# Kernel optimization log

Measured on AMD Instinct MI355X. Metric: run time of the kernel, lower is better.

The kernel has to match this reference:

```python
import jax, jax.numpy as jnp
import numpy as np

N_HEADS = 16


def setup_inputs() -> dict:
    key = jax.random.key(0)
    ks = jax.random.split(key, 11)
    B, S, D = 4, 2048, 1024
    scale = 1.0 / np.sqrt(D)
    inp = {
        "xq": jax.random.normal(ks[0], (B, S, D), jnp.float32),
        "xk": jax.random.normal(ks[1], (B, S, D), jnp.float32),
        "xv": jax.random.normal(ks[2], (B, S, D), jnp.float32),
        "wq": jax.random.normal(ks[3], (D, D), jnp.float32) * scale,
        "bq": jnp.zeros((D,), jnp.float32),
        "wk": jax.random.normal(ks[4], (D, D), jnp.float32) * scale,
        "bk": jnp.zeros((D,), jnp.float32),
        "wv": jax.random.normal(ks[5], (D, D), jnp.float32) * scale,
        "bv": jnp.zeros((D,), jnp.float32),
        "wo": jax.random.normal(ks[6], (D, D), jnp.float32) * scale,
        "bo": jnp.zeros((D,), jnp.float32),
    }
    return inp


def reference(xq, xk, xv, wq, bq, wk, bk, wv, bv, wo, bo):
    B, S, D = xq.shape
    H = N_HEADS
    dh = D // H

    def split_heads(x):
        # (B, S, D) -> (B, H, S, dh)
        return x.reshape(B, S, H, dh).transpose(0, 2, 1, 3)

    q = split_heads(xq @ wq + bq)
    k = split_heads(xk @ wk + bk)
    v = split_heads(xv @ wv + bv)

    # FFT-based autocorrelation along the sequence axis (axis=2)
    q_fft = jnp.fft.rfft(q, axis=2)
    k_fft = jnp.fft.rfft(k, axis=2)
    autocorr = jnp.fft.irfft(q_fft * jnp.conj(k_fft), n=S, axis=2)  # (B,H,S,dh)
    scaled = autocorr / jnp.sqrt(jnp.float32(dh))

    # top-k delay selection over mean correlation across channel dim
    k_top = max(S // 5, 1)
    mean_corr = scaled.mean(axis=-1)  # (B,H,S)
    top_values, top_indices = jax.lax.top_k(mean_corr, k_top)  # (B,H,K)

    # gather values at top delays: (B,H,K,dh)
    v_sel = jnp.take_along_axis(v, top_indices[..., None], axis=2)
    weights = jax.nn.softmax(top_values, axis=-1)  # (B,H,K)
    attended = jnp.einsum('bhk,bhkd->bhd', weights, v_sel)  # (B,H,dh)

    # broadcast across seq, merge heads, output projection
    out = jnp.broadcast_to(attended[:, :, None, :], (B, H, S, dh))
    out = out.transpose(0, 2, 1, 3).reshape(B, S, D)
    return out @ wo + bo
```

## Files before the change

kernel.cpp:

```cpp
#include <hip/hip_runtime.h>
#include <math.h>

#define SB 4
#define SS 2048
#define SD 1024
#define SH 16
#define KTOP 409
#define KSL 8
#define KPS 52

typedef float f32x4  __attribute__((ext_vector_type(4)));
typedef short bf16x8 __attribute__((ext_vector_type(8)));
typedef short s16x4  __attribute__((ext_vector_type(4)));

__device__ __forceinline__ short f2bf(float x) {
  unsigned u = __float_as_uint(x);
  u += 0x7fff + ((u >> 16) & 1);
  return (short)(u >> 16);
}
__device__ __forceinline__ float bf2f(short s) {
  return __uint_as_float(((unsigned)(unsigned short)s) << 16);
}

__device__ __forceinline__ void gld16(const void* g, void* l) {
  __builtin_amdgcn_global_load_lds(
      (const __attribute__((address_space(1))) void*)g,
      (__attribute__((address_space(3))) void*)l, 16, 0, 0);
}

#define XS(i) ((i) ^ (((i) >> 4) & 15))

template<int SIGN>
__device__ __forceinline__ void fft2048_lds(float2* z, const float2* tw, int tid) {
#pragma unroll
  for (int l = 0; l < 4; ++l) {
    int bf = tid + l * 256;
    int i0 = XS(2 * bf), i1 = XS(2 * bf + 1);
    float2 a = z[i0], b = z[i1];
    z[i0] = make_float2(a.x + b.x, a.y + b.y);
    z[i1] = make_float2(a.x - b.x, a.y - b.y);
  }
  __syncthreads();
#pragma unroll
  for (int lq = 1; lq <= 9; lq += 2) {
    const int q = 1 << lq;
#pragma unroll
    for (int l = 0; l < 2; ++l) {
      int bf = tid + l * 256;
      int p = bf & (q - 1);
      int base = ((bf >> lq) << (lq + 2)) + p;
      int e1 = p << (9 - lq);
      int e2 = e1 << 1;
      int e3 = e1 * 3;
      float2 w1 = tw[XS(e1)];
      float2 w2 = tw[XS(e2)];
      float s3 = 1.f; int e3w = e3;
      if (e3 >= 1024) { e3w = e3 - 1024; s3 = -1.f; }
      float2 w3 = tw[XS(e3w)]; w3.x *= s3; w3.y *= s3;
      float2 t0 = z[XS(base)];
      float2 vb = z[XS(base + 2 * q)];
      float2 vc = z[XS(base + q)];
      float2 vd = z[XS(base + 3 * q)];
      float w1i = SIGN * w1.y, w2i = SIGN * w2.y, w3i = SIGN * w3.y;
      float2 t1 = make_float2(vb.x * w1.x - vb.y * w1i, vb.x * w1i + vb.y * w1.x);
      float2 t2 = make_float2(vc.x * w2.x - vc.y * w2i, vc.x * w2i + vc.y * w2.x);
      float2 t3 = make_float2(vd.x * w3.x - vd.y * w3i, vd.x * w3i + vd.y * w3.x);
      float2 s02 = make_float2(t0.x + t2.x, t0.y + t2.y);
      float2 d02 = make_float2(t0.x - t2.x, t0.y - t2.y);
      float2 s13 = make_float2(t1.x + t3.x, t1.y + t3.y);
      float2 d13 = make_float2(t1.x - t3.x, t1.y - t3.y);
      float2 r13 = make_float2(SIGN * d13.y, -SIGN * d13.x);
      z[XS(base)]         = make_float2(s02.x + s13.x, s02.y + s13.y);
      z[XS(base + q)]     = make_float2(d02.x + r13.x, d02.y + r13.y);
      z[XS(base + 2 * q)] = make_float2(s02.x - s13.x, s02.y - s13.y);
      z[XS(base + 3 * q)] = make_float2(d02.x - r13.x, d02.y - r13.y);
    }
    __syncthreads();
  }
}

template<int SIGN>
__device__ __forceinline__ void fft2048x2_lds(
    float2* __restrict__ z0, float2* __restrict__ z1,
    const float2* tw, int tid)
{
#pragma unroll
  for (int l = 0; l < 4; ++l) {
    int bf = tid + l * 256;
    int i0 = XS(2 * bf), i1 = XS(2 * bf + 1);
    float2 a0 = z0[i0], b0 = z0[i1];
    float2 a1 = z1[i0], b1 = z1[i1];
    z0[i0] = make_float2(a0.x + b0.x, a0.y + b0.y);
    z0[i1] = make_float2(a0.x - b0.x, a0.y - b0.y);
    z1[i0] = make_float2(a1.x + b1.x, a1.y + b1.y);
    z1[i1] = make_float2(a1.x - b1.x, a1.y - b1.y);
  }
  __syncthreads();
#pragma unroll
  for (int lq = 1; lq <= 9; lq += 2) {
    const int q = 1 << lq;
#pragma unroll
    for (int l = 0; l < 2; ++l) {
      int bf = tid + l * 256;
      int p = bf & (q - 1);
      int base = ((bf >> lq) << (lq + 2)) + p;
      int e1 = p << (9 - lq);
      int e2 = e1 << 1;
      int e3 = e1 * 3;
      float2 w1 = tw[XS(e1)];
      float2 w2 = tw[XS(e2)];
      float s3 = 1.f; int e3w = e3;
      if (e3 >= 1024) { e3w = e3 - 1024; s3 = -1.f; }
      float2 w3 = tw[XS(e3w)]; w3.x *= s3; w3.y *= s3;
      float w1i = SIGN * w1.y, w2i = SIGN * w2.y, w3i = SIGN * w3.y;
      const int ia = XS(base), ib = XS(base + 2 * q),
                ic = XS(base + q), id = XS(base + 3 * q);
#pragma unroll
      for (int s = 0; s < 2; ++s) {
        float2* z = s ? z1 : z0;
        float2 t0 = z[ia];
        float2 vb = z[ib];
        float2 vc = z[ic];
        float2 vd = z[id];
        float2 t1 = make_float2(vb.x * w1.x - vb.y * w1i, vb.x * w1i + vb.y * w1.x);
        float2 t2 = make_float2(vc.x * w2.x - vc.y * w2i, vc.x * w2i + vc.y * w2.x);
        float2 t3 = make_float2(vd.x * w3.x - vd.y * w3i, vd.x * w3i + vd.y * w3.x);
        float2 s02 = make_float2(t0.x + t2.x, t0.y + t2.y);
        float2 d02 = make_float2(t0.x - t2.x, t0.y - t2.y);
        float2 s13 = make_float2(t1.x + t3.x, t1.y + t3.y);
        float2 d13 = make_float2(t1.x - t3.x, t1.y - t3.y);
        float2 r13 = make_float2(SIGN * d13.y, -SIGN * d13.x);
        z[ia] = make_float2(s02.x + s13.x, s02.y + s13.y);
        z[ic] = make_float2(d02.x + r13.x, d02.y + r13.y);
        z[ib] = make_float2(s02.x - s13.x, s02.y - s13.y);
        z[id] = make_float2(d02.x - r13.x, d02.y - r13.y);
      }
    }
    __syncthreads();
  }
}

__global__ __launch_bounds__(256) void twiddle_k(float2* __restrict__ twtab) {
  int j = blockIdx.x * 256 + threadIdx.x;
  float a = 6.2831853071795864769f * (float)j / 2048.0f;
  twtab[j] = make_float2(cosf(a), -sinf(a));
}

__global__ __launch_bounds__(256) void splitwt_k(
    const float* __restrict__ wq, const float* __restrict__ wk,
    short* __restrict__ wqt, short* __restrict__ wkt)
{
  const float* W = blockIdx.z ? wk : wq;
  short* Wt = blockIdx.z ? wkt : wqt;
  const int n0 = blockIdx.x * 64, k0 = blockIdx.y * 64;
  __shared__ float T[64][65];
  const int tid = threadIdx.x;
#pragma unroll
  for (int l = 0; l < 4; ++l) {
    int idx = tid + l * 256;
    int r = idx >> 4, c4 = (idx & 15) << 2;
    float4 v = *(const float4*)&W[(size_t)(k0 + r) * SD + n0 + c4];
    T[r][c4 + 0] = v.x; T[r][c4 + 1] = v.y; T[r][c4 + 2] = v.z; T[r][c4 + 3] = v.w;
  }
  __syncthreads();
#pragma unroll
  for (int l = 0; l < 4; ++l) {
    int idx = tid + l * 256;
    int nr = idx >> 4, k4 = (idx & 15) << 2;
    s16x4 hi, lo;
#pragma unroll
    for (int j = 0; j < 4; ++j) {
      float x = T[k4 + j][nr];
      short hb = f2bf(x);
      hi[j] = hb; lo[j] = f2bf(x - bf2f(hb));
    }
    int ks = (((k4 >> 3) ^ (nr & 7)) << 3) | (k4 & 7);
    *(s16x4*)&Wt[(size_t)(n0 + nr) * 2048 + k0 + ks] = hi;
    *(s16x4*)&Wt[(size_t)(n0 + nr) * 2048 + 1024 + k0 + ks] = lo;
  }
}

__global__ __launch_bounds__(256) void splitx2_k(
    const float* __restrict__ Xq, const float* __restrict__ Xk,
    short* __restrict__ Xqh, short* __restrict__ Xql,
    short* __restrict__ Xkh, short* __restrict__ Xkl)
{
  const int tid = threadIdx.x;
  const int row = blockIdx.x * 2 + (tid >> 7);
  const int G = tid & 127;
  const float* X = blockIdx.y ? Xk : Xq;
  short* Xh = blockIdx.y ? Xkh : Xqh;
  short* Xl = blockIdx.y ? Xkl : Xql;
  const float* src = X + ((size_t)row << 10) + (G << 3);
  float4 a = *(const float4*)src;
  float4 b = *(const float4*)(src + 4);
  float xs[8] = {a.x, a.y, a.z, a.w, b.x, b.y, b.z, b.w};
  bf16x8 hi, lo;
#pragma unroll
  for (int j = 0; j < 8; ++j) {
    short hb = f2bf(xs[j]);
    hi[j] = hb; lo[j] = f2bf(xs[j] - bf2f(hb));
  }
  int Gd = (G & 0x78) | ((G ^ row) & 7);
  size_t d = ((size_t)row << 10) + (Gd << 3);
  *(bf16x8*)&Xh[d] = hi;
  *(bf16x8*)&Xl[d] = lo;
}

__global__ __launch_bounds__(256) void projm_k(
    const short* __restrict__ Xh, const short* __restrict__ Xl,
    const short* __restrict__ Wt, const float* __restrict__ bias,
    float* __restrict__ Out, int ldT)
{
  const int n0 = blockIdx.x * 128, m0 = blockIdx.y * 128;
  __shared__ __align__(16) short Ah[128 * 64];
  __shared__ __align__(16) short Al[128 * 64];
  __shared__ __align__(16) short Bh[128 * 64];
  __shared__ __align__(16) short Bl[128 * 64];
  const int tid = threadIdx.x;
  const int wave = tid >> 6, lane = tid & 63, l15 = lane & 15, kq = lane >> 4;
  const int wr = wave >> 1, wc = wave & 1;
  const int sr = lane >> 3, sc = lane & 7;
  f32x4 acc[4][4];
#pragma unroll
  for (int i = 0; i < 4; ++i)
#pragma unroll
    for (int j = 0; j < 4; ++j)
#pragma unroll
      for (int r = 0; r < 4; ++r) acc[i][j][r] = 0.f;
  float bval[4];
#pragma unroll
  for (int j = 0; j < 4; ++j) bval[j] = bias[n0 + wc * 64 + j * 16 + l15];

  for (int s = 0; s < 16; ++s) {
    __syncthreads();
#pragma unroll
    for (int l = 0; l < 4; ++l) {
      int rr = l * 32 + wave * 8 + sr;
      int lofs = (l * 32 + wave * 8) * 64;
      size_t gA = ((size_t)(m0 + rr) << 10) + (s << 6) + (sc << 3);
      gld16(Xh + gA, Ah + lofs);
      gld16(Xl + gA, Al + lofs);
      size_t gB = ((size_t)(n0 + rr) << 11) + (s << 6) + (sc << 3);
      gld16(Wt + gB, Bh + lofs);
      gld16(Wt + gB + 1024, Bl + lofs);
    }
    __syncthreads();
#pragma unroll
    for (int ks = 0; ks < 2; ++ks) {
      int seg = ks * 4 + kq;
      bf16x8 ah[4], al[4], bh[4], bl[4];
#pragma unroll
      for (int i = 0; i < 4; ++i) {
        int ar = wr * 64 + i * 16 + l15;
        int addr = ar * 64 + ((seg ^ (ar & 7)) << 3);
        ah[i] = *(const bf16x8*)&Ah[addr];
        al[i] = *(const bf16x8*)&Al[addr];
      }
#pragma unroll
      for (int j = 0; j < 4; ++j) {
        int br = wc * 64 + j * 16 + l15;
        int addr = br * 64 + ((seg ^ (br & 7)) << 3);
        bh[j] = *(const bf16x8*)&Bh[addr];
        bl[j] = *(const bf16x8*)&Bl[addr];
      }
#pragma unroll
      for (int i = 0; i < 4; ++i)
#pragma unroll
        for (int j = 0; j < 4; ++j) {
          acc[i][j] = __builtin_amdgcn_mfma_f32_16x16x32_bf16(ah[i], bh[j], acc[i][j], 0, 0, 0);
          acc[i][j] = __builtin_amdgcn_mfma_f32_16x16x32_bf16(al[i], bh[j], acc[i][j], 0, 0, 0);
          acc[i][j] = __builtin_amdgcn_mfma_f32_16x16x32_bf16(ah[i], bl[j], acc[i][j], 0, 0, 0);
        }
    }
  }
#pragma unroll
  for (int i = 0; i < 4; ++i)
#pragma unroll
    for (int j = 0; j < 4; ++j) {
      int n = n0 + wc * 64 + j * 16 + l15;
      int tb = m0 + wr * 64 + i * 16 + kq * 4;
      float4 v = make_float4(acc[i][j][0] + bval[j], acc[i][j][1] + bval[j],
                             acc[i][j][2] + bval[j], acc[i][j][3] + bval[j]);
      *(float4*)&Out[(size_t)n * ldT + tb] = v;
    }
}

__global__ __launch_bounds__(256) void fftcorr_k(
    const float* __restrict__ Qt, const float* __restrict__ Kt,
    float* __restrict__ P, const float2* __restrict__ twtab, int ld)
{
  const int dg = blockIdx.x, h = blockIdx.y, b = blockIdx.z;
  float* Pb = P + (size_t)b * SH * SS * 2;
  const size_t bofs = (size_t)b * SS;
  __shared__ float2 z0[2048];
  __shared__ float2 z1[2048];
  __shared__ float2 tw[1024];
  const int tid = threadIdx.x;
  for (int j = tid; j < 1024; j += 256) tw[XS(j)] = twtab[j];

  const int n = h * 64 + dg * 2;
  const float* q0 = Qt + (size_t)n * ld + bofs;
  const float* k0 = Kt + (size_t)n * ld + bofs;
  const float* q1 = q0 + ld;
  const float* k1 = k0 + ld;
#pragma unroll
  for (int l = 0; l < 8; ++l) {
    int t = tid + l * 256;
    int rv = __brev((unsigned)t) >> 21;
    z0[XS(rv)] = make_float2(q0[t], k0[t]);
    z1[XS(rv)] = make_float2(q1[t], k1[t]);
  }
  __syncthreads();
  fft2048x2_lds<1>(z0, z1, tw, tid);
#pragma unroll
  for (int l = 0; l < 8; ++l) {
    int f = tid + l * 256;
    int fc = (2048 - f) & 2047;
    float prr = 0.f, pii = 0.f;
#pragma unroll
    for (int s = 0; s < 2; ++s) {
      const float2* z = s ? z1 : z0;
      float2 Z = z[XS(f)];
      float2 Zc = z[XS(fc)];
      float Zcr = Zc.x, Zci = -Zc.y;
      float Qr = 0.5f * (Z.x + Zcr), Qi = 0.5f * (Z.y + Zci);
      float Kr = 0.5f * (Z.y - Zci), Ki = -0.5f * (Z.x - Zcr);
      prr += Qr * Kr + Qi * Ki;
      pii += Qi * Kr - Qr * Ki;
    }
    atomicAdd(&Pb[((size_t)h * SS + f) * 2 + 0], prr);
    atomicAdd(&Pb[((size_t)h * SS + f) * 2 + 1], pii);
  }
}

__global__ __launch_bounds__(256) void ifft_topk_k(
    const float* __restrict__ P, const float2* __restrict__ twtab,
    int* __restrict__ sidx, float* __restrict__ sw)
{
  const int bh = blockIdx.x;
  __shared__ float2 z[2048];
  __shared__ float2 tw[1024];
  __shared__ unsigned keys[2048];
  __shared__ int el_i[KTOP];
  __shared__ float el_w[KTOP];
  __shared__ int hist[256];
  __shared__ int scan_sh[256];
  __shared__ int cnt2, tiecnt, sel_v;
  __shared__ unsigned kmax_sh;
  __shared__ float Zsh;
  const int tid = threadIdx.x;
  const float SCL = 1.0f / (2048.0f * 512.0f);

  for (int j = tid; j < 1024; j += 256) tw[XS(j)] = twtab[j];
  if (tid == 0) { cnt2 = 0; tiecnt = 0; kmax_sh = 0u; Zsh = 0.f; }
#pragma unroll
  for (int l = 0; l < 8; ++l) {
    int f = tid + l * 256;
    int rv = __brev((unsigned)f) >> 21;
    z[XS(rv)] = make_float2(P[((size_t)bh * SS + f) * 2 + 0],
                            P[((size_t)bh * SS + f) * 2 + 1]);
  }
  __syncthreads();
  fft2048_lds<-1>(z, tw, tid);

  unsigned lm = 0u;
#pragma unroll
  for (int l = 0; l < 8; ++l) {
    int i = tid + l * 256;
    float v = z[XS(i)].x * SCL;
    z[XS(i)].x = v;
    unsigned u = __float_as_uint(v);
    unsigned k = (u & 0x80000000u) ? ~u : (u | 0x80000000u);
    keys[i] = k;
    lm = max(lm, k);
  }
  atomicMax(&kmax_sh, lm);
  __syncthreads();

  unsigned prefix = 0u;
  int remaining = KTOP;
  for (int p = 3; p >= 0; --p) {
    hist[tid] = 0;
    __syncthreads();
    unsigned mask_hi = (p == 3) ? 0u : (0xFFFFFFFFu << ((p + 1) * 8));
#pragma unroll
    for (int l = 0; l < 8; ++l) {
      unsigned k = keys[tid + l * 256];
      if ((k & mask_hi) == prefix) atomicAdd(&hist[(k >> (p * 8)) & 255], 1);
    }
    __syncthreads();
    scan_sh[tid] = hist[tid];
    __syncthreads();
    for (int off = 1; off < 256; off <<= 1) {
      int add = (tid + off < 256) ? scan_sh[tid + off] : 0;
      __syncthreads();
      scan_sh[tid] += add;
      __syncthreads();
    }
    if (scan_sh[tid] >= remaining && (tid == 255 || scan_sh[tid + 1] < remaining))
      sel_v = tid;
    __syncthreads();
    int v = sel_v;
    int above = (v == 255) ? 0 : scan_sh[v + 1];
    remaining -= above;
    prefix |= ((unsigned)v) << (p * 8);
    __syncthreads();
  }
  const unsigned T = prefix;
  unsigned km = kmax_sh;
  float vmax = __uint_as_float((km & 0x80000000u) ? (km ^ 0x80000000u) : ~km);

#pragma unroll
  for (int l = 0; l < 8; ++l) {
    int i = tid + l * 256;
    unsigned k = keys[i];
    if (k > T) {
      int pos = atomicAdd(&cnt2, 1);
      el_i[pos] = i;
      el_w[pos] = expf(z[XS(i)].x - vmax);
    } else if (k == T) {
      atomicAdd(&tiecnt, 1);
    }
  }
  __syncthreads();
  int need = KTOP - cnt2;
  if (tiecnt == need) {
#pragma unroll
    for (int l = 0; l < 8; ++l) {
      int i = tid + l * 256;
      if (keys[i] == T) {
        int pos = atomicAdd(&cnt2, 1);
        el_i[pos] = i;
        el_w[pos] = expf(z[XS(i)].x - vmax);
      }
    }
  } else if (tid == 0) {
    int pos = cnt2;
    for (int i = 0; i < SS && pos < KTOP; ++i)
      if (keys[i] == T) { el_i[pos] = i; el_w[pos] = expf(z[XS(i)].x - vmax); ++pos; }
  }
  __syncthreads();
  float zs = 0.f;
  for (int l = tid; l < KTOP; l += 256) zs += el_w[l];
  atomicAdd(&Zsh, zs);
  __syncthreads();
  float invZ = 1.0f / Zsh;
  for (int l = tid; l < KTOP; l += 256) {
    sidx[bh * KTOP + l] = el_i[l];
    sw[bh * KTOP + l]   = el_w[l] * invZ;
  }
}

__global__ __launch_bounds__(256) void xbar_k(
    const int* __restrict__ sidx, const float* __restrict__ sw,
    const float* __restrict__ xv, float* __restrict__ xbar)
{
  const int bh = blockIdx.x, b = bh >> 4, sl = blockIdx.y;
  const int r0 = sl * KPS;
  const int r1 = min(KTOP, r0 + KPS);
  __shared__ int il[KPS];
  __shared__ float wl[KPS];
  const int tid = threadIdx.x;
  if (tid < r1 - r0) {
    il[tid] = sidx[bh * KTOP + r0 + tid];
    wl[tid] = sw[bh * KTOP + r0 + tid];
  }
  __syncthreads();
  const float4* xv4 = (const float4*)xv;
  float4 acc = make_float4(0.f, 0.f, 0.f, 0.f);
  for (int r = 0; r < r1 - r0; ++r) {
    float w = wl[r];
    float4 v = xv4[(size_t)(b * SS + il[r]) * 256 + tid];
    acc.x += w * v.x; acc.y += w * v.y; acc.z += w * v.z; acc.w += w * v.w;
  }
  float* dst = xbar + (size_t)bh * 1024 + tid * 4;
  atomicAdd(dst + 0, acc.x); atomicAdd(dst + 1, acc.y);
  atomicAdd(dst + 2, acc.z); atomicAdd(dst + 3, acc.w);
}

__global__ __launch_bounds__(256) void initbias_k(
    const float* __restrict__ bv, const float* __restrict__ bo,
    float* __restrict__ att, float* __restrict__ orow)
{
  int i = blockIdx.x * 256 + threadIdx.x;
  if (i < 4096) att[i] = bv[i & 1023];
  else          orow[i - 4096] = bo[i & 1023];
}

__global__ __launch_bounds__(256) void attend_k(
    const float* __restrict__ xbar, const float* __restrict__ wv,
    float* __restrict__ att)
{
  const int b = blockIdx.y, i0 = blockIdx.x * 64;
  __shared__ float xs[16 * 64];
  const int tid = threadIdx.x;
#pragma unroll
  for (int l = 0; l < 4; ++l) {
    int f = tid + l * 256;
    xs[f] = xbar[(size_t)(b * 16 + (f >> 6)) * 1024 + i0 + (f & 63)];
  }
  __syncthreads();
  const float4* wv4 = (const float4*)wv;
  const int h = tid >> 4;
  float4 acc = make_float4(0.f, 0.f, 0.f, 0.f);
  for (int m = 0; m < 64; ++m) {
    float xvs = xs[h * 64 + m];
    float4 w = wv4[(size_t)(i0 + m) * 256 + tid];
    acc.x += xvs * w.x; acc.y += xvs * w.y; acc.z += xvs * w.z; acc.w += xvs * w.w;
  }
  float* dst = att + (size_t)b * 1024 + tid * 4;
  atomicAdd(dst + 0, acc.x); atomicAdd(dst + 1, acc.y);
  atomicAdd(dst + 2, acc.z); atomicAdd(dst + 3, acc.w);
}

__global__ __launch_bounds__(256) void oproj_k(
    const float* __restrict__ att, const float* __restrict__ wo,
    float* __restrict__ orow)
{
  const int b = blockIdx.y, m0 = blockIdx.x * 64;
  __shared__ float as_[64];
  const int tid = threadIdx.x;
  if (tid < 64) as_[tid] = att[(size_t)b * 1024 + m0 + tid];
  __syncthreads();
  const float4* wo4 = (const float4*)wo;
  float4 acc = make_float4(0.f, 0.f, 0.f, 0.f);
  for (int m = 0; m < 64; ++m) {
    float a = as_[m];
    float4 w = wo4[(size_t)(m0 + m) * 256 + tid];
    acc.x += a * w.x; acc.y += a * w.y; acc.z += a * w.z; acc.w += a * w.w;
  }
  float* dst = orow + (size_t)b * 1024 + tid * 4;
  atomicAdd(dst + 0, acc.x); atomicAdd(dst + 1, acc.y);
  atomicAdd(dst + 2, acc.z); atomicAdd(dst + 3, acc.w);
}

__global__ __launch_bounds__(256) void bcast_k(
    const float* __restrict__ orow, float* __restrict__ out)
{
  int idx = blockIdx.x * 256 + threadIdx.x;
  const float4* o4 = (const float4*)orow;
  ((float4*)out)[idx] = o4[((idx >> 19) << 8) | (idx & 255)];
}

extern "C" void kernel_launch(void* const* d_in, const int* in_sizes, int n_in,
                              void* d_out, int out_size, void* d_ws, size_t ws_size,
                              hipStream_t stream) {
  (void)in_sizes; (void)n_in; (void)out_size;
  const float* xq = (const float*)d_in[0];
  const float* xk = (const float*)d_in[1];
  const float* xv = (const float*)d_in[2];
  const float* wq = (const float*)d_in[3];
  const float* bq = (const float*)d_in[4];
  const float* wk = (const float*)d_in[5];
  const float* bk = (const float*)d_in[6];
  const float* wv = (const float*)d_in[7];
  const float* bv = (const float*)d_in[8];
  const float* wo = (const float*)d_in[9];
  const float* bo = (const float*)d_in[10];
  float* out = (float*)d_out;

  char* base = (char*)d_ws;
  float* P = (float*)base;
  size_t off = (size_t)SB * SH * SS * 2 * 4;
  float2* twtab = (float2*)(base + off); off += 1024 * 8;
  int*   sidx = (int*)  (base + off); off += (size_t)SB * SH * KTOP * 4;
  float* sw   = (float*)(base + off); off += (size_t)SB * SH * KTOP * 4;
  float* xbar = (float*)(base + off); off += (size_t)SB * SH * SD * 4;
  float* att  = (float*)(base + off); off += (size_t)SB * SD * 4;
  float* orow = (float*)(base + off); off += (size_t)SB * SD * 4;

  size_t big0 = (off + 1048575) & ~(size_t)1048575;
  const size_t SZ_X = (size_t)SB * SS * SD * 2;
  const size_t SZ_T = (size_t)SD * SB * SS * 4;
  const size_t SZ_W = (size_t)SD * 2048 * 2;
  size_t need_big = big0 + 4 * SZ_X + 2 * SZ_T + 2 * SZ_W;

  twiddle_k<<<dim3(4), 256, 0, stream>>>(twtab);
  hipMemsetAsync(P, 0, (size_t)SB * SH * SS * 2 * sizeof(float), stream);
  hipMemsetAsync(xbar, 0, (size_t)SB * SH * SD * sizeof(float), stream);

  if (ws_size >= need_big) {
    char* bb = base + big0;
    short* Xqh = (short*)(bb);
    short* Xql = (short*)(bb + SZ_X);
    short* Xkh = (short*)(bb + 2 * SZ_X);
    short* Xkl = (short*)(bb + 3 * SZ_X);
    float* Qt  = (float*)(bb + 4 * SZ_X);
    float* Kt  = (float*)(bb + 4 * SZ_X + SZ_T);
    short* Wqt = (short*)(bb + 4 * SZ_X + 2 * SZ_T);
    short* Wkt = (short*)(bb + 4 * SZ_X + 2 * SZ_T + SZ_W);

    splitwt_k<<<dim3(16, 16, 2), 256, 0, stream>>>(wq, wk, Wqt, Wkt);
    splitx2_k<<<dim3(SB * SS / 2, 2), 256, 0, stream>>>(xq, xk, Xqh, Xql, Xkh, Xkl);
    projm_k<<<dim3(8, SB * SS / 128), 256, 0, stream>>>(Xqh, Xql, Wqt, bq, Qt, SB * SS);
    projm_k<<<dim3(8, SB * SS / 128), 256, 0, stream>>>(Xkh, Xkl, Wkt, bk, Kt, SB * SS);
    fftcorr_k<<<dim3(32, 16, SB), 256, 0, stream>>>(Qt, Kt, P, twtab, SB * SS);
  } else {
    char* ob = (char*)d_out;
    float* Qt  = (float*)(ob);
    float* Kt  = (float*)(ob + ( 8u << 20));
    short* Wqt = (short*)(ob + (16u << 20));
    short* Wkt = (short*)(ob + (20u << 20));
    short* Xh  = (short*)(ob + (24u << 20));
    short* Xl  = (short*)(ob + (28u << 20));

    splitwt_k<<<dim3(16, 16, 2), 256, 0, stream>>>(wq, wk, Wqt, Wkt);
    for (int b = 0; b < SB; ++b) {
      const float* xqb = xq + (size_t)b * SS * SD;
      const float* xkb = xk + (size_t)b * SS * SD;
      splitx2_k<<<dim3(SS / 2, 1), 256, 0, stream>>>(xqb, xqb, Xh, Xl, Xh, Xl);
      projm_k<<<dim3(8, SS / 128), 256, 0, stream>>>(Xh, Xl, Wqt, bq, Qt, SS);
      splitx2_k<<<dim3(SS / 2, 1), 256, 0, stream>>>(xkb, xkb, Xh, Xl, Xh, Xl);
      projm_k<<<dim3(8, SS / 128), 256, 0, stream>>>(Xh, Xl, Wkt, bk, Kt, SS);
      fftcorr_k<<<dim3(32, 16, 1), 256, 0, stream>>>(
          Qt, Kt, P + (size_t)b * SH * SS * 2, twtab, SS);
    }
  }

  ifft_topk_k<<<dim3(SB * SH), 256, 0, stream>>>(P, twtab, sidx, sw);
  xbar_k<<<dim3(SB * SH, KSL), 256, 0, stream>>>(sidx, sw, xv, xbar);
  initbias_k<<<dim3(32), 256, 0, stream>>>(bv, bo, att, orow);
  attend_k<<<dim3(16, SB), 256, 0, stream>>>(xbar, wv, att);
  oproj_k<<<dim3(16, SB), 256, 0, stream>>>(att, wo, orow);
  bcast_k<<<dim3(8192), 256, 0, stream>>>(orow, out);
}
```

Baseline: 397.0 us.

## Batch Q/K projections, replace FFT atomics with partials, warp-shuffle scan

Merges the Q and K projection GEMMs into one launch using blockIdx.z. fftcorr now has each block process 8 channels instead of 2, with vectorized float2 loads, and writes per-group partial spectra that ifft_topk sums in place of global atomics. That also drops the P memset. The LDS swizzle gains a higher-bit XOR to cut bank conflicts, and the radix-select prefix scan uses wavefront shuffles instead of a barrier-heavy Hillis-Steele loop. The cost is fewer fftcorr blocks (lower parallelism) and an extra partial-spectrum buffer.

```diff
diff --git a/kernel.cpp b/kernel.cpp
--- a/kernel.cpp
+++ b/kernel.cpp
@@ -28,7 +28,7 @@
       (__attribute__((address_space(3))) void*)l, 16, 0, 0);
 }
 
-#define XS(i) ((i) ^ (((i) >> 4) & 15))
+#define XS(i) ((i) ^ ((((i) >> 4) ^ ((i) >> 8)) & 15))
 
 template<int SIGN>
 __device__ __forceinline__ void fft2048_lds(float2* z, const float2* tw, int tid) {
@@ -208,10 +208,16 @@
 }
 
 __global__ __launch_bounds__(256) void projm_k(
-    const short* __restrict__ Xh, const short* __restrict__ Xl,
-    const short* __restrict__ Wt, const float* __restrict__ bias,
-    float* __restrict__ Out, int ldT)
-{
+    const short* __restrict__ Xqh, const short* __restrict__ Xql,
+    const short* __restrict__ Wq_, const float* __restrict__ bq_,
+    float* __restrict__ Oq_,
+    const short* __restrict__ Xkh, const short* __restrict__ Xkl,
+    const short* __restrict__ Wk_, const float* __restrict__ bk_,
+    float* __restrict__ Ok_, int ldT)
+{
+  const short* Xh; const short* Xl; const short* Wt; const float* bias; float* Out;
+  if (blockIdx.z == 0) { Xh = Xqh; Xl = Xql; Wt = Wq_; bias = bq_; Out = Oq_; }
+  else                 { Xh = Xkh; Xl = Xkl; Wt = Wk_; bias = bk_; Out = Ok_; }
   const int n0 = blockIdx.x * 128, m0 = blockIdx.y * 128;
   __shared__ __align__(16) short Ah[128 * 64];
   __shared__ __align__(16) short Al[128 * 64];
@@ -288,54 +294,81 @@
 
 __global__ __launch_bounds__(256) void fftcorr_k(
     const float* __restrict__ Qt, const float* __restrict__ Kt,
-    float* __restrict__ P, const float2* __restrict__ twtab, int ld)
+    float* __restrict__ Pat, float2* __restrict__ Ppart,
+    const float2* __restrict__ twtab, int ld)
 {
   const int dg = blockIdx.x, h = blockIdx.y, b = blockIdx.z;
-  float* Pb = P + (size_t)b * SH * SS * 2;
   const size_t bofs = (size_t)b * SS;
   __shared__ float2 z0[2048];
   __shared__ float2 z1[2048];
   __shared__ float2 tw[1024];
   const int tid = threadIdx.x;
   for (int j = tid; j < 1024; j += 256) tw[XS(j)] = twtab[j];
-
-  const int n = h * 64 + dg * 2;
-  const float* q0 = Qt + (size_t)n * ld + bofs;
-  const float* k0 = Kt + (size_t)n * ld + bofs;
-  const float* q1 = q0 + ld;
-  const float* k1 = k0 + ld;
-#pragma unroll
-  for (int l = 0; l < 8; ++l) {
-    int t = tid + l * 256;
-    int rv = __brev((unsigned)t) >> 21;
-    z0[XS(rv)] = make_float2(q0[t], k0[t]);
-    z1[XS(rv)] = make_float2(q1[t], k1[t]);
-  }
-  __syncthreads();
-  fft2048x2_lds<1>(z0, z1, tw, tid);
-#pragma unroll
-  for (int l = 0; l < 8; ++l) {
-    int f = tid + l * 256;
-    int fc = (2048 - f) & 2047;
-    float prr = 0.f, pii = 0.f;
-#pragma unroll
-    for (int s = 0; s < 2; ++s) {
-      const float2* z = s ? z1 : z0;
-      float2 Z = z[XS(f)];
-      float2 Zc = z[XS(fc)];
-      float Zcr = Zc.x, Zci = -Zc.y;
-      float Qr = 0.5f * (Z.x + Zcr), Qi = 0.5f * (Z.y + Zci);
-      float Kr = 0.5f * (Z.y - Zci), Ki = -0.5f * (Z.x - Zcr);
-      prr += Qr * Kr + Qi * Ki;
-      pii += Qi * Kr - Qr * Ki;
-    }
-    atomicAdd(&Pb[((size_t)h * SS + f) * 2 + 0], prr);
-    atomicAdd(&Pb[((size_t)h * SS + f) * 2 + 1], pii);
+  float prr[8], pii[8];
+#pragma unroll
+  for (int l = 0; l < 8; ++l) { prr[l] = 0.f; pii[l] = 0.f; }
+
+  for (int dd = 0; dd < 4; ++dd) {
+    const int n = h * 64 + dg * 8 + dd * 2;
+    const float2* q0 = (const float2*)(Qt + (size_t)n * ld + bofs);
+    const float2* k0 = (const float2*)(Kt + (size_t)n * ld + bofs);
+    const float2* q1 = (const float2*)(Qt + (size_t)(n + 1) * ld + bofs);
+    const float2* k1 = (const float2*)(Kt + (size_t)(n + 1) * ld + bofs);
+    __syncthreads();
+#pragma unroll
+    for (int l = 0; l < 4; ++l) {
+      int t2 = tid + l * 256;
+      int t = 2 * t2;
+      int rv = __brev((unsigned)t) >> 21;
+      int zia = XS(rv);
+      int zib = XS(rv + 1024);
+      float2 fq0 = q0[t2], fk0 = k0[t2];
+      float2 fq1 = q1[t2], fk1 = k1[t2];
+      z0[zia] = make_float2(fq0.x, fk0.x);
+      z0[zib] = make_float2(fq0.y, fk0.y);
+      z1[zia] = make_float2(fq1.x, fk1.x);
+      z1[zib] = make_float2(fq1.y, fk1.y);
+    }
+    __syncthreads();
+    fft2048x2_lds<1>(z0, z1, tw, tid);
+#pragma unroll
+    for (int l = 0; l < 8; ++l) {
+      int f = tid + l * 256;
+      int fc = (2048 - f) & 2047;
+#pragma unroll
+      for (int s = 0; s < 2; ++s) {
+        const float2* z = s ? z1 : z0;
+        float2 Z = z[XS(f)];
+        float2 Zc = z[XS(fc)];
+        float Zcr = Zc.x, Zci = -Zc.y;
+        float Qr = 0.5f * (Z.x + Zcr), Qi = 0.5f * (Z.y + Zci);
+        float Kr = 0.5f * (Z.y - Zci), Ki = -0.5f * (Z.x - Zcr);
+        prr[l] += Qr * Kr + Qi * Ki;
+        pii[l] += Qi * Kr - Qr * Ki;
+      }
+    }
+  }
+  if (Ppart) {
+    float2* Pp = Ppart + ((size_t)dg * 64 + (size_t)b * SH + h) * 2048;
+#pragma unroll
+    for (int l = 0; l < 8; ++l) {
+      int f = tid + l * 256;
+      Pp[f] = make_float2(prr[l], pii[l]);
+    }
+  } else {
+    float* Pb = Pat;
+#pragma unroll
+    for (int l = 0; l < 8; ++l) {
+      int f = tid + l * 256;
+      atomicAdd(&Pb[((size_t)h * SS + f) * 2 + 0], prr[l]);
+      atomicAdd(&Pb[((size_t)h * SS + f) * 2 + 1], pii[l]);
+    }
   }
 }
 
 __global__ __launch_bounds__(256) void ifft_topk_k(
-    const float* __restrict__ P, const float2* __restrict__ twtab,
+    const float* __restrict__ P, const float2* __restrict__ Ppart, int nparts,
+    const float2* __restrict__ twtab,
     int* __restrict__ sidx, float* __restrict__ sw)
 {
   const int bh = blockIdx.x;
@@ -346,10 +379,12 @@
   __shared__ float el_w[KTOP];
   __shared__ int hist[256];
   __shared__ int scan_sh[256];
+  __shared__ int wtot[4];
   __shared__ int cnt2, tiecnt, sel_v;
   __shared__ unsigned kmax_sh;
   __shared__ float Zsh;
   const int tid = threadIdx.x;
+  const int lane = tid & 63, wv = tid >> 6;
   const float SCL = 1.0f / (2048.0f * 512.0f);
 
   for (int j = tid; j < 1024; j += 256) tw[XS(j)] = twtab[j];
@@ -358,8 +393,17 @@
   for (int l = 0; l < 8; ++l) {
     int f = tid + l * 256;
     int rv = __brev((unsigned)f) >> 21;
-    z[XS(rv)] = make_float2(P[((size_t)bh * SS + f) * 2 + 0],
-                            P[((size_t)bh * SS + f) * 2 + 1]);
+    float2 acc;
+    if (nparts > 0) {
+      acc = make_float2(0.f, 0.f);
+      for (int g = 0; g < nparts; ++g) {
+        float2 v = Ppart[((size_t)g * 64 + bh) * 2048 + f];
+        acc.x += v.x; acc.y += v.y;
+      }
+    } else {
+      acc = ((const float2*)P)[(size_t)bh * SS + f];
+    }
+    z[XS(rv)] = acc;
   }
   __syncthreads();
   fft2048_lds<-1>(z, tw, tid);
@@ -390,21 +434,24 @@
       if ((k & mask_hi) == prefix) atomicAdd(&hist[(k >> (p * 8)) & 255], 1);
     }
     __syncthreads();
-    scan_sh[tid] = hist[tid];
-    __syncthreads();
-    for (int off = 1; off < 256; off <<= 1) {
-      int add = (tid + off < 256) ? scan_sh[tid + off] : 0;
-      __syncthreads();
-      scan_sh[tid] += add;
-      __syncthreads();
-    }
+    int v = hist[tid];
+#pragma unroll
+    for (int off2 = 1; off2 < 64; off2 <<= 1) {
+      int t = __shfl_down(v, off2);
+      if (lane + off2 < 64) v += t;
+    }
+    if (lane == 0) wtot[wv] = v;
+    __syncthreads();
+    for (int w = wv + 1; w < 4; ++w) v += wtot[w];
+    scan_sh[tid] = v;
+    __syncthreads();
     if (scan_sh[tid] >= remaining && (tid == 255 || scan_sh[tid + 1] < remaining))
       sel_v = tid;
     __syncthreads();
-    int v = sel_v;
-    int above = (v == 255) ? 0 : scan_sh[v + 1];
+    int vsel = sel_v;
+    int above = (vsel == 255) ? 0 : scan_sh[vsel + 1];
     remaining -= above;
-    prefix |= ((unsigned)v) << (p * 8);
+    prefix |= ((unsigned)vsel) << (p * 8);
     __syncthreads();
   }
   const unsigned T = prefix;
@@ -574,10 +621,10 @@
   const size_t SZ_X = (size_t)SB * SS * SD * 2;
   const size_t SZ_T = (size_t)SD * SB * SS * 4;
   const size_t SZ_W = (size_t)SD * 2048 * 2;
-  size_t need_big = big0 + 4 * SZ_X + 2 * SZ_T + 2 * SZ_W;
+  const size_t SZ_P = (size_t)8 * 64 * 2048 * 8;
+  size_t need_big = big0 + 4 * SZ_X + 2 * SZ_T + 2 * SZ_W + SZ_P;
 
   twiddle_k<<<dim3(4), 256, 0, stream>>>(twtab);
-  hipMemsetAsync(P, 0, (size_t)SB * SH * SS * 2 * sizeof(float), stream);
   hipMemsetAsync(xbar, 0, (size_t)SB * SH * SD * sizeof(float), stream);
 
   if (ws_size >= need_big) {
@@ -590,12 +637,15 @@
     float* Kt  = (float*)(bb + 4 * SZ_X + SZ_T);
     short* Wqt = (short*)(bb + 4 * SZ_X + 2 * SZ_T);
     short* Wkt = (short*)(bb + 4 * SZ_X + 2 * SZ_T + SZ_W);
+    float2* Pp = (float2*)(bb + 4 * SZ_X + 2 * SZ_T + 2 * SZ_W);
 
     splitwt_k<<<dim3(16, 16, 2), 256, 0, stream>>>(wq, wk, Wqt, Wkt);
     splitx2_k<<<dim3(SB * SS / 2, 2), 256, 0, stream>>>(xq, xk, Xqh, Xql, Xkh, Xkl);
-    projm_k<<<dim3(8, SB * SS / 128), 256, 0, stream>>>(Xqh, Xql, Wqt, bq, Qt, SB * SS);
-    projm_k<<<dim3(8, SB * SS / 128), 256, 0, stream>>>(Xkh, Xkl, Wkt, bk, Kt, SB * SS);
-    fftcorr_k<<<dim3(32, 16, SB), 256, 0, stream>>>(Qt, Kt, P, twtab, SB * SS);
+    projm_k<<<dim3(8, SB * SS / 128, 2), 256, 0, stream>>>(
+        Xqh, Xql, Wqt, bq, Qt, Xkh, Xkl, Wkt, bk, Kt, SB * SS);
+    fftcorr_k<<<dim3(8, 16, SB), 256, 0, stream>>>(
+        Qt, Kt, nullptr, Pp, twtab, SB * SS);
+    ifft_topk_k<<<dim3(SB * SH), 256, 0, stream>>>(P, Pp, 8, twtab, sidx, sw);
   } else {
     char* ob = (char*)d_out;
     float* Qt  = (float*)(ob);
@@ -605,20 +655,23 @@
     short* Xh  = (short*)(ob + (24u << 20));
     short* Xl  = (short*)(ob + (28u << 20));
 
+    hipMemsetAsync(P, 0, (size_t)SB * SH * SS * 2 * sizeof(float), stream);
     splitwt_k<<<dim3(16, 16, 2), 256, 0, stream>>>(wq, wk, Wqt, Wkt);
     for (int b = 0; b < SB; ++b) {
       const float* xqb = xq + (size_t)b * SS * SD;
       const float* xkb = xk + (size_t)b * SS * SD;
       splitx2_k<<<dim3(SS / 2, 1), 256, 0, stream>>>(xqb, xqb, Xh, Xl, Xh, Xl);
-      projm_k<<<dim3(8, SS / 128), 256, 0, stream>>>(Xh, Xl, Wqt, bq, Qt, SS);
+      projm_k<<<dim3(8, SS / 128, 1), 256, 0, stream>>>(
+          Xh, Xl, Wqt, bq, Qt, Xh, Xl, Wqt, bq, Qt, SS);
       splitx2_k<<<dim3(SS / 2, 1), 256, 0, stream>>>(xkb, xkb, Xh, Xl, Xh, Xl);
-      projm_k<<<dim3(8, SS / 128), 256, 0, stream>>>(Xh, Xl, Wkt, bk, Kt, SS);
-      fftcorr_k<<<dim3(32, 16, 1), 256, 0, stream>>>(
-          Qt, Kt, P + (size_t)b * SH * SS * 2, twtab, SS);
-    }
-  }
-
-  ifft_topk_k<<<dim3(SB * SH), 256, 0, stream>>>(P, twtab, sidx, sw);
+      projm_k<<<dim3(8, SS / 128, 1), 256, 0, stream>>>(
+          Xh, Xl, Wkt, bk, Kt, Xh, Xl, Wkt, bk, Kt, SS);
+      fftcorr_k<<<dim3(8, 16, 1), 256, 0, stream>>>(
+          Qt, Kt, P + (size_t)b * SH * SS * 2, nullptr, twtab, SS);
+    }
+    ifft_topk_k<<<dim3(SB * SH), 256, 0, stream>>>(P, nullptr, 0, twtab, sidx, sw);
+  }
+
   xbar_k<<<dim3(SB * SH, KSL), 256, 0, stream>>>(sidx, sw, xv, xbar);
   initbias_k<<<dim3(32), 256, 0, stream>>>(bv, bo, att, orow);
   attend_k<<<dim3(16, SB), 256, 0, stream>>>(xbar, wv, att);
```

Result: faster. 381.2 us (-4.0%).
